# Performance work log

Measured on AMD Instinct MI355X. Metric: run time of the kernel, lower is better.

## Reference

```python
import jax, jax.numpy as jnp
import numpy as np

L, D, H, HK, DH, F, V, T, B = 8, 1024, 16, 4, 64, 2816, 32000, 1024, 2
G = H // HK
THETA = 10000.0
EPS = 1e-6
SCALE = DH ** -0.5


def _rope_tables(t, dh, theta):
    inv = 1.0 / theta ** (jnp.arange(0, dh, 2, dtype=jnp.float32) / dh)  # [dh/2]
    ang = jnp.arange(t, dtype=jnp.float32)[:, None] * inv[None, :]       # [T, dh/2]
    return jnp.cos(ang), jnp.sin(ang)


def _apply_rope(x, cos, sin):
    # x: [B, T, h, DH] -> rotate pairs (even, odd)
    xr = x.reshape(*x.shape[:-1], DH // 2, 2)
    x0, x1 = xr[..., 0], xr[..., 1]
    c = cos[None, :, None, :]
    s = sin[None, :, None, :]
    out = jnp.stack([x0 * c - x1 * s, x0 * s + x1 * c], axis=-1)
    return out.reshape(*x.shape)


def _rmsnorm(x, w):
    var = jnp.mean(x * x, axis=-1, keepdims=True)
    return x * jax.lax.rsqrt(var + EPS) * w


def setup_inputs() -> dict:
    key = jax.random.key(0)
    ks = jax.random.split(key, 10)
    s = 0.02
    return {
        "ids": jax.random.randint(ks[0], (B, T), 0, V),
        "emb": jax.random.normal(ks[1], (V, D), jnp.float32) * s,
        "qw": jax.random.normal(ks[2], (L, H * DH, D), jnp.float32) * s,
        "kw": jax.random.normal(ks[3], (L, HK * DH, D), jnp.float32) * s,
        "vw": jax.random.normal(ks[4], (L, HK * DH, D), jnp.float32) * s,
        "ow": jax.random.normal(ks[5], (L, D, D), jnp.float32) * s,
        "w1": jax.random.normal(ks[6], (L, F, D), jnp.float32) * s,
        "w2": jax.random.normal(ks[7], (L, D, F), jnp.float32) * s,
        "w3": jax.random.normal(ks[8], (L, F, D), jnp.float32) * s,
        "n1": jnp.ones((L, D), jnp.float32),
        "n2": jnp.ones((L, D), jnp.float32),
        "nf": jnp.ones((D,), jnp.float32),
    }


def _forward(ids, emb, qw, kw, vw, ow, w1, w2, w3, n1, n2, nf):
    cos, sin = _rope_tables(T, DH, THETA)
    causal = jnp.tril(jnp.ones((T, T), dtype=bool))  # [T, T]
    x = emb[ids]  # [B, T, D]
    for l in range(L):
        xn = _rmsnorm(x, n1[l])
        q = jnp.einsum("btd,ed->bte", xn, qw[l]).reshape(B, T, H, DH)
        k = jnp.einsum("btd,ed->bte", xn, kw[l]).reshape(B, T, HK, DH)
        v = jnp.einsum("btd,ed->bte", xn, vw[l]).reshape(B, T, HK, DH)
        q = _apply_rope(q, cos, sin)
        k = _apply_rope(k, cos, sin)
        # GQA: group query heads over shared kv heads
        qg = q.transpose(0, 2, 1, 3).reshape(B, HK, G, T, DH)
        kh = k.transpose(0, 2, 1, 3)  # [B, HK, T, DH]
        vh = v.transpose(0, 2, 1, 3)
        scores = jnp.einsum("bkgtd,bksd->bkgts", qg, kh) * SCALE
        scores = jnp.where(causal, scores, -jnp.inf)
        p = jax.nn.softmax(scores, axis=-1)
        out = jnp.einsum("bkgts,bksd->bkgtd", p, vh)
        out = out.reshape(B, H, T, DH).transpose(0, 2, 1, 3).reshape(B, T, D)
        x = x + jnp.einsum("btd,ed->bte", out, ow[l])
        xn2 = _rmsnorm(x, n2[l])
        h1 = jnp.einsum("btd,fd->btf", xn2, w1[l])
        h3 = jnp.einsum("btd,fd->btf", xn2, w3[l])
        x = x + jnp.einsum("btf,df->btd", jax.nn.silu(h1) * h3, w2[l])
    x = _rmsnorm(x, nf)
    logits = jnp.einsum("btd,vd->btv", x, emb)  # tied lm_head
    return logits


def reference(ids, emb, qw, kw, vw, ow, w1, w2, w3, n1, n2, nf):
    return _forward(ids, emb, qw, kw, vw, ow, w1, w2, w3, n1, n2, nf)
```

## Files before the change

kernel.cpp:

```cpp
#include <hip/hip_runtime.h>
#include <math.h>

#define L_ 8
#define D_ 1024
#define H_ 16
#define HK_ 4
#define DH_ 64
#define F_ 2816
#define V_ 32000
#define T_ 1024
#define B_ 2
#define M_ (B_*T_)
#define SCALE_ 0.125f

typedef unsigned short u16;
typedef unsigned int   u32;
typedef __attribute__((ext_vector_type(4))) float  f32x4;
typedef __attribute__((ext_vector_type(8))) short  bf16x8;
typedef __attribute__((ext_vector_type(4))) unsigned short u16x4;
typedef __attribute__((ext_vector_type(4))) unsigned int   u32x4;

__device__ __forceinline__ float bf2f(u16 h) {
    union { u32 u; float f; } v; v.u = ((u32)h) << 16; return v.f;
}
__device__ __forceinline__ u16 f2bf(float f) {
    union { float f; u32 u; } v; v.f = f;
    u32 r = v.u + 0x7fffu + ((v.u >> 16) & 1u);
    return (u16)(r >> 16);
}

__device__ __forceinline__ void gl_lds16(const void* g, void* l) {
    __builtin_amdgcn_global_load_lds(
        (const __attribute__((address_space(1))) unsigned int*)g,
        (__attribute__((address_space(3))) unsigned int*)l,
        16, 0, 0);
}

template<int BM, int EPI>
__global__ __launch_bounds__(256)
void gemm2_k(const u16* __restrict__ A, int K,
             const u16* __restrict__ W, int N,
             float* __restrict__ Of, u16* __restrict__ Ob)
{
    constexpr int FM = BM / 32;
    constexpr int FN = 4;
    constexpr int GM = M_ / BM;
    constexpr int IPA = BM / 64;
    __shared__ u16 sA[2 * BM * 32];
    __shared__ u16 sB[2 * 128 * 32];

    const int tid  = threadIdx.x;
    const int lane = tid & 63, wv = tid >> 6;
    const int wm = wv >> 1, wn = wv & 1;
    const int l15 = lane & 15, lhi = lane >> 4;
    const int m0 = wm * (BM / 2), n0 = wn * 64;

    const int nwg = gridDim.x;
    const int q8 = nwg >> 3, r8 = nwg & 7;
    const int xcd = blockIdx.x & 7, off8 = blockIdx.x >> 3;
    const int wgid = (xcd < r8 ? xcd * (q8 + 1) : r8 * (q8 + 1) + (xcd - r8) * q8) + off8;
    const int tM = wgid % GM, tN = wgid / GM;

    const int srow = lane >> 2;
    const int scol = (lane & 3) * 8;

    const u16* Abase = A + (size_t)(tM * BM) * K;
    const u16* Wbase = W + (size_t)(tN * 128) * K;

    f32x4 acc[FM][FN];
#pragma unroll
    for (int i = 0; i < FM; ++i)
#pragma unroll
        for (int j = 0; j < FN; ++j) acc[i][j] = f32x4{0.f, 0.f, 0.f, 0.f};

    auto stage = [&](int kt, int buf) {
        u16* sa = sA + buf * (BM * 32);
        u16* sb = sB + buf * (128 * 32);
#pragma unroll
        for (int i = 0; i < IPA; ++i) {
            int c = wv * IPA + i;
            gl_lds16(Abase + (size_t)(c * 16 + srow) * K + kt + scol, sa + c * 512);
        }
#pragma unroll
        for (int i = 0; i < 2; ++i) {
            int c = wv * 2 + i;
            gl_lds16(Wbase + (size_t)(c * 16 + srow) * K + kt + scol, sb + c * 512);
        }
    };

    const int nt = K >> 5;
    stage(0, 0);
    asm volatile("s_waitcnt vmcnt(0)" ::: "memory");
    __syncthreads();

    int cur = 0;
    for (int t = 0; t < nt; ++t) {
        if (t + 1 < nt) stage((t + 1) << 5, cur ^ 1);

        const u16* sa = sA + cur * (BM * 32);
        const u16* sb = sB + cur * (128 * 32);
        bf16x8 av[FM], bv[FN];
#pragma unroll
        for (int i = 0; i < FM; ++i)
            av[i] = *(const bf16x8*)&sa[(m0 + i * 16 + l15) * 32 + lhi * 8];
#pragma unroll
        for (int j = 0; j < FN; ++j)
            bv[j] = *(const bf16x8*)&sb[(n0 + j * 16 + l15) * 32 + lhi * 8];
#pragma unroll
        for (int i = 0; i < FM; ++i)
#pragma unroll
            for (int j = 0; j < FN; ++j)
                acc[i][j] = __builtin_amdgcn_mfma_f32_16x16x32_bf16(
                    av[i], bv[j], acc[i][j], 0, 0, 0);

        if (t + 1 < nt) {
            asm volatile("s_waitcnt vmcnt(0)" ::: "memory");
            __syncthreads();
            cur ^= 1;
        }
    }

#pragma unroll
    for (int i = 0; i < FM; ++i)
#pragma unroll
        for (int j = 0; j < FN; ++j) {
            size_t gm = (size_t)tM * BM + m0 + i * 16 + lhi * 4;
            size_t gn = (size_t)tN * 128 + n0 + j * 16 + l15;
#pragma unroll
            for (int r = 0; r < 4; ++r) {
                float v = acc[i][j][r];
                size_t idx = (gm + r) * (size_t)N + gn;
                if (EPI == 0)      Ob[idx] = f2bf(v);
                else if (EPI == 1) Of[idx] = v;
                else               Of[idx] += v;
            }
        }
}

__global__ __launch_bounds__(256)
void cvt_k(const float* __restrict__ src, u16* __restrict__ dst,
           unsigned long long sStride, unsigned long long dStride)
{
    int l = blockIdx.y;
    size_t i = ((size_t)blockIdx.x * 256 + threadIdx.x) * 4;
    f32x4 v = *(const f32x4*)(src + l * sStride + i);
    u16x4 o;
    o.x = f2bf(v.x); o.y = f2bf(v.y); o.z = f2bf(v.z); o.w = f2bf(v.w);
    *(u16x4*)(dst + l * dStride + i) = o;
}

template<int BM, int BN, int EPI, int NW>
__global__ __launch_bounds__(256)
void gemm_k(const u16* __restrict__ A, int K,
            const float* __restrict__ W0, const float* __restrict__ W1p,
            const float* __restrict__ W2p, int N0, int N1, int N,
            float* __restrict__ Of, u16* __restrict__ Ob)
{
    constexpr int FM = BM / 32;
    constexpr int FN = BN / 32;
    constexpr int LS = 40;
    __shared__ u16 sA[BM * LS];
    __shared__ u16 sB[BN * LS];

    const int tid  = threadIdx.x;
    const int lane = tid & 63, wv = tid >> 6;
    const int wm = wv >> 1, wn = wv & 1;
    const int l15 = lane & 15, lhi = lane >> 4;
    const int m0 = wm * (BM / 2), n0 = wn * (BN / 2);
    const int tM = blockIdx.y, tN = blockIdx.x;

    f32x4 acc[FM][FN];
#pragma unroll
    for (int i = 0; i < FM; ++i)
#pragma unroll
        for (int j = 0; j < FN; ++j) acc[i][j] = f32x4{0.f, 0.f, 0.f, 0.f};

    for (int kt = 0; kt < K; kt += 32) {
#pragma unroll
        for (int i = 0; i < BM / 64; ++i) {
            int cid = tid + i * 256;
            int row = cid >> 2, kc = cid & 3;
            const u16* src = A + (size_t)(tM * BM + row) * K + kt + kc * 8;
            *(u32x4*)&sA[row * LS + kc * 8] = *(const u32x4*)src;
        }
#pragma unroll
        for (int i = 0; i < BN / 32; ++i) {
            int cid = tid + i * 256;
            int row = cid >> 3, kc = cid & 7;
            int n = tN * BN + row;
            const float* wr;
            if (NW == 1)      wr = W0 + (size_t)n * K;
            else if (NW == 2) wr = (n < N0) ? (W0 + (size_t)n * K)
                                            : (W1p + (size_t)(n - N0) * K);
            else              wr = (n < N0) ? (W0 + (size_t)n * K)
                               : (n < N0 + N1) ? (W1p + (size_t)(n - N0) * K)
                                               : (W2p + (size_t)(n - N0 - N1) * K);
            f32x4 v = *(const f32x4*)(wr + kt + kc * 4);
            u16x4 o;
            o.x = f2bf(v.x); o.y = f2bf(v.y); o.z = f2bf(v.z); o.w = f2bf(v.w);
            *(u16x4*)&sB[row * LS + kc * 4] = o;
        }
        __syncthreads();

        bf16x8 av[FM], bv[FN];
#pragma unroll
        for (int i = 0; i < FM; ++i)
            av[i] = *(const bf16x8*)&sA[(m0 + i * 16 + l15) * LS + lhi * 8];
#pragma unroll
        for (int j = 0; j < FN; ++j)
            bv[j] = *(const bf16x8*)&sB[(n0 + j * 16 + l15) * LS + lhi * 8];
#pragma unroll
        for (int i = 0; i < FM; ++i)
#pragma unroll
            for (int j = 0; j < FN; ++j)
                acc[i][j] = __builtin_amdgcn_mfma_f32_16x16x32_bf16(
                    av[i], bv[j], acc[i][j], 0, 0, 0);
        __syncthreads();
    }

#pragma unroll
    for (int i = 0; i < FM; ++i)
#pragma unroll
        for (int j = 0; j < FN; ++j) {
            size_t gm = (size_t)tM * BM + m0 + i * 16 + lhi * 4;
            size_t gn = (size_t)tN * BN + n0 + j * 16 + l15;
#pragma unroll
            for (int r = 0; r < 4; ++r) {
                float v = acc[i][j][r];
                size_t idx = (gm + r) * (size_t)N + gn;
                if (EPI == 0)      Ob[idx] = f2bf(v);
                else if (EPI == 1) Of[idx] = v;
                else               Of[idx] += v;
            }
        }
}

__global__ __launch_bounds__(256)
void attn_k(const u16* __restrict__ qkv, u16* __restrict__ attn)
{
    const int qt = blockIdx.x, h = blockIdx.y, b = blockIdx.z;
    const int hk = h >> 2;
    const int tid = threadIdx.x;
    const int lane = tid & 63, w = tid >> 6;
    const int l15 = lane & 15, lhi = lane >> 4;
    __shared__ u16 sK[64 * 72];
    __shared__ u16 sVT[64 * 72];
    __shared__ u16 sP[4 * 16 * 72];

    const int q0 = qt * 64;
    const u16* qptr = qkv + (size_t)(b * T_ + q0 + w * 16 + l15) * 1536 + h * 64 + lhi * 8;
    bf16x8 aq0 = *(const bf16x8*)qptr;
    bf16x8 aq1 = *(const bf16x8*)(qptr + 32);

    f32x4 accO[4];
#pragma unroll
    for (int d = 0; d < 4; ++d) accO[d] = f32x4{0.f, 0.f, 0.f, 0.f};
    float m_r[4] = {-1e30f, -1e30f, -1e30f, -1e30f};
    float l_r[4] = {0.f, 0.f, 0.f, 0.f};
    const int myq = q0 + w * 16 + lhi * 4;
    u16* sPw = sP + w * 16 * 72;

    for (int kt = 0; kt <= qt; ++kt) {
#pragma unroll
        for (int i = 0; i < 2; ++i) {
            int cid = tid + i * 256;
            int r = cid >> 3, kc = cid & 7;
            const u16* src = qkv + (size_t)(b * T_ + kt * 64 + r) * 1536 + 1024 + hk * 64 + kc * 8;
            *(u32x4*)&sK[r * 72 + kc * 8] = *(const u32x4*)src;
        }
#pragma unroll
        for (int i = 0; i < 2; ++i) {
            int cid = tid + i * 256;
            int tt = cid >> 3, dc = cid & 7;
            const u16* src = qkv + (size_t)(b * T_ + kt * 64 + tt) * 1536 + 1280 + hk * 64 + dc * 8;
            bf16x8 vv = *(const bf16x8*)src;
#pragma unroll
            for (int j = 0; j < 8; ++j) sVT[(dc * 8 + j) * 72 + tt] = (u16)vv[j];
        }
        __syncthreads();

        f32x4 accS[4];
#pragma unroll
        for (int nf = 0; nf < 4; ++nf) accS[nf] = f32x4{0.f, 0.f, 0.f, 0.f};
#pragma unroll
        for (int s = 0; s < 2; ++s) {
            bf16x8 aqs = s ? aq1 : aq0;
#pragma unroll
            for (int nf = 0; nf < 4; ++nf) {
                bf16x8 bk = *(const bf16x8*)&sK[(nf * 16 + l15) * 72 + s * 32 + lhi * 8];
                accS[nf] = __builtin_amdgcn_mfma_f32_16x16x32_bf16(aqs, bk, accS[nf], 0, 0, 0);
            }
        }
#pragma unroll
        for (int nf = 0; nf < 4; ++nf)
#pragma unroll
            for (int r = 0; r < 4; ++r) {
                float v = accS[nf][r] * SCALE_;
                if (kt == qt) {
                    int kp = kt * 64 + nf * 16 + l15;
                    if (kp > myq + r) v = -1e30f;
                }
                accS[nf][r] = v;
            }
        float sc[4];
#pragma unroll
        for (int r = 0; r < 4; ++r) {
            float mx = fmaxf(fmaxf(accS[0][r], accS[1][r]), fmaxf(accS[2][r], accS[3][r]));
#pragma unroll
            for (int off = 1; off < 16; off <<= 1) mx = fmaxf(mx, __shfl_xor(mx, off));
            float mn = fmaxf(m_r[r], mx);
            sc[r] = expf(m_r[r] - mn);
            m_r[r] = mn;
        }
        float rs[4] = {0.f, 0.f, 0.f, 0.f};
#pragma unroll
        for (int nf = 0; nf < 4; ++nf)
#pragma unroll
            for (int r = 0; r < 4; ++r) {
                float p = expf(accS[nf][r] - m_r[r]);
                accS[nf][r] = p;
                rs[r] += p;
            }
#pragma unroll
        for (int r = 0; r < 4; ++r) {
#pragma unroll
            for (int off = 1; off < 16; off <<= 1) rs[r] += __shfl_xor(rs[r], off);
            l_r[r] = l_r[r] * sc[r] + rs[r];
        }
#pragma unroll
        for (int d = 0; d < 4; ++d)
#pragma unroll
            for (int r = 0; r < 4; ++r) accO[d][r] *= sc[r];

#pragma unroll
        for (int nf = 0; nf < 4; ++nf)
#pragma unroll
            for (int r = 0; r < 4; ++r)
                sPw[(lhi * 4 + r) * 72 + nf * 16 + l15] = f2bf(accS[nf][r]);
        bf16x8 pa0 = *(const bf16x8*)&sPw[l15 * 72 + lhi * 8];
        bf16x8 pa1 = *(const bf16x8*)&sPw[l15 * 72 + 32 + lhi * 8];
#pragma unroll
        for (int s = 0; s < 2; ++s) {
            bf16x8 pas = s ? pa1 : pa0;
#pragma unroll
            for (int d = 0; d < 4; ++d) {
                bf16x8 bvv = *(const bf16x8*)&sVT[(d * 16 + l15) * 72 + s * 32 + lhi * 8];
                accO[d] = __builtin_amdgcn_mfma_f32_16x16x32_bf16(pas, bvv, accO[d], 0, 0, 0);
            }
        }
        __syncthreads();
    }

#pragma unroll
    for (int d = 0; d < 4; ++d)
#pragma unroll
        for (int r = 0; r < 4; ++r) {
            int row = q0 + w * 16 + lhi * 4 + r;
            float o = accO[d][r] / l_r[r];
            attn[(size_t)(b * T_ + row) * 1024 + h * 64 + d * 16 + l15] = f2bf(o);
        }
}

__global__ __launch_bounds__(256)
void gather_k(const int* __restrict__ ids, const float* __restrict__ emb,
              float* __restrict__ x)
{
    int m = blockIdx.x, tid = threadIdx.x;
    int id = ids[m];
    *(f32x4*)(x + (size_t)m * D_ + tid * 4) =
        *(const f32x4*)(emb + (size_t)id * D_ + tid * 4);
}

__global__ __launch_bounds__(256)
void rmsnorm_k(const float* __restrict__ x, const float* __restrict__ g,
               u16* __restrict__ out)
{
    const int row = blockIdx.x, tid = threadIdx.x;
    const float* xr = x + (size_t)row * D_;
    f32x4 v = *(const f32x4*)(xr + tid * 4);
    float ss = v.x * v.x + v.y * v.y + v.z * v.z + v.w * v.w;
#pragma unroll
    for (int off = 32; off >= 1; off >>= 1) ss += __shfl_xor(ss, off);
    __shared__ float red[4];
    if ((tid & 63) == 0) red[tid >> 6] = ss;
    __syncthreads();
    float tot = red[0] + red[1] + red[2] + red[3];
    float rr = rsqrtf(tot * (1.0f / D_) + 1e-6f);
    f32x4 wv = *(const f32x4*)(g + tid * 4);
    u16x4 o;
    o.x = f2bf(v.x * rr * wv.x); o.y = f2bf(v.y * rr * wv.y);
    o.z = f2bf(v.z * rr * wv.z); o.w = f2bf(v.w * rr * wv.w);
    *(u16x4*)(out + (size_t)row * D_ + tid * 4) = o;
}

__global__ __launch_bounds__(256)
void rope_tab_k(float* __restrict__ tc, float* __restrict__ ts)
{
    int idx = blockIdx.x * 256 + threadIdx.x;
    int t = idx >> 5, j = idx & 31;
    float inv = powf(10000.0f, -(float)j * (1.0f / 32.0f));
    float ang = (float)t * inv;
    tc[idx] = cosf(ang);
    ts[idx] = sinf(ang);
}

__global__ __launch_bounds__(256)
void rope_k(u16* __restrict__ qkv, const float* __restrict__ tc,
            const float* __restrict__ ts)
{
    int idx = blockIdx.x * 256 + threadIdx.x;
    int m = idx / 160;
    int c = idx - m * 160;
    int t = m & (T_ - 1);
    int col = (c < 128) ? (c * 8) : (1024 + (c - 128) * 8);
    int j0 = (col & 63) >> 1;
    f32x4 cv = *(const f32x4*)(tc + t * 32 + j0);
    f32x4 sv = *(const f32x4*)(ts + t * 32 + j0);
    u16* p = qkv + (size_t)m * 1536 + col;
    bf16x8 v = *(const bf16x8*)p;
    bf16x8 o;
#pragma unroll
    for (int i = 0; i < 4; ++i) {
        float x0 = bf2f((u16)v[2 * i]), x1 = bf2f((u16)v[2 * i + 1]);
        o[2 * i]     = (short)f2bf(x0 * cv[i] - x1 * sv[i]);
        o[2 * i + 1] = (short)f2bf(x0 * sv[i] + x1 * cv[i]);
    }
    *(bf16x8*)p = o;
}

__global__ __launch_bounds__(256)
void silu_k(const u16* __restrict__ h13, u16* __restrict__ hh)
{
    int idx = blockIdx.x * 256 + threadIdx.x;
    int m = idx / 352;
    int c = idx - m * 352;
    const u16* h1p = h13 + (size_t)m * (2 * F_) + c * 8;
    bf16x8 a = *(const bf16x8*)h1p;
    bf16x8 b = *(const bf16x8*)(h1p + F_);
    bf16x8 o;
#pragma unroll
    for (int j = 0; j < 8; ++j) {
        float av = bf2f((u16)a[j]);
        float s = av / (1.0f + expf(-av));
        o[j] = (short)f2bf(s * bf2f((u16)b[j]));
    }
    *(bf16x8*)(hh + (size_t)m * F_ + c * 8) = o;
}

__global__ __launch_bounds__(256)
void silu_f32_k(const float* __restrict__ h13, u16* __restrict__ hh)
{
    int m = blockIdx.y;
    int f = blockIdx.x * 256 + threadIdx.x;
    float a = h13[(size_t)m * (2 * F_) + f];
    float c = h13[(size_t)m * (2 * F_) + F_ + f];
    float s = a / (1.0f + expf(-a));
    hh[(size_t)m * F_ + f] = f2bf(s * c);
}

__global__ __launch_bounds__(640)
void rope_slow_k(u16* __restrict__ qkv)
{
    int m = blockIdx.x;
    int c2 = threadIdx.x;
    int col = (c2 < 512) ? (c2 * 2) : (1024 + (c2 - 512) * 2);
    int d = col & 63;
    int t = m & (T_ - 1);
    float ang = (float)t * powf(10000.0f, -(float)d / 64.0f);
    float cs = cosf(ang), sn = sinf(ang);
    u16* p = qkv + (size_t)m * 1536 + col;
    float x0 = bf2f(p[0]), x1 = bf2f(p[1]);
    p[0] = f2bf(x0 * cs - x1 * sn);
    p[1] = f2bf(x0 * sn + x1 * cs);
}

extern "C" void kernel_launch(void* const* d_in, const int* in_sizes, int n_in,
                              void* d_out, int out_size, void* d_ws, size_t ws_size,
                              hipStream_t stream)
{
    const int*   ids = (const int*)d_in[0];
    const float* emb = (const float*)d_in[1];
    const float* qw  = (const float*)d_in[2];
    const float* kw  = (const float*)d_in[3];
    const float* vw  = (const float*)d_in[4];
    const float* ow  = (const float*)d_in[5];
    const float* w1  = (const float*)d_in[6];
    const float* w2  = (const float*)d_in[7];
    const float* w3  = (const float*)d_in[8];
    const float* n1  = (const float*)d_in[9];
    const float* n2  = (const float*)d_in[10];
    const float* nfw = (const float*)d_in[11];
    float* out = (float*)d_out;
    char*  ws  = (char*)d_ws;

    float* x    = (float*)(ws);
    u16*   xn   = (u16*)(ws + 8388608ULL);
    u16*   qkvb = (u16*)(ws + 12582912ULL);
    u16*   attnb= (u16*)(ws + 18874368ULL);
    u16*   h13  = (u16*)(ws + 23068672ULL);
    u16*   hh   = (u16*)(ws + 46137344ULL);
    float* ropec= (float*)(ws + 57671680ULL);
    float* ropes= (float*)(ws + 57802752ULL);
    u16*   embb = (u16*)(ws + 57933824ULL);
    u16*   wqkv = (u16*)(ws + 123469824ULL);
    u16*   wob  = (u16*)(ws + 148635648ULL);
    u16*   w13b = (u16*)(ws + 165412864ULL);
    u16*   w2b  = (u16*)(ws + 257687552ULL);
    const unsigned long long NEED = 303824896ULL;

    if (ws_size >= NEED) {
        cvt_k<<<dim3(32000, 1), 256, 0, stream>>>(emb, embb, 0, 0);
        cvt_k<<<dim3(1024, L_), 256, 0, stream>>>(qw, wqkv,            1048576ULL, 1572864ULL);
        cvt_k<<<dim3(256,  L_), 256, 0, stream>>>(kw, wqkv + 1048576,  262144ULL,  1572864ULL);
        cvt_k<<<dim3(256,  L_), 256, 0, stream>>>(vw, wqkv + 1310720,  262144ULL,  1572864ULL);
        cvt_k<<<dim3(1024, L_), 256, 0, stream>>>(ow, wob,             1048576ULL, 1048576ULL);
        cvt_k<<<dim3(2816, L_), 256, 0, stream>>>(w1, w13b,            2883584ULL, 5767168ULL);
        cvt_k<<<dim3(2816, L_), 256, 0, stream>>>(w3, w13b + 2883584,  2883584ULL, 5767168ULL);
        cvt_k<<<dim3(2816, L_), 256, 0, stream>>>(w2, w2b,             2883584ULL, 2883584ULL);
        rope_tab_k<<<T_ * 32 / 256, 256, 0, stream>>>(ropec, ropes);

        gather_k<<<M_, 256, 0, stream>>>(ids, emb, x);

        for (int l = 0; l < L_; ++l) {
            rmsnorm_k<<<M_, 256, 0, stream>>>(x, n1 + l * D_, xn);
            gemm2_k<64, 0><<<32 * 12, 256, 0, stream>>>(
                xn, D_, wqkv + (size_t)l * 1572864, 1536, nullptr, qkvb);
            rope_k<<<M_ * 160 / 256, 256, 0, stream>>>(qkvb, ropec, ropes);
            attn_k<<<dim3(T_ / 64, H_, B_), 256, 0, stream>>>(qkvb, attnb);
            gemm2_k<64, 2><<<32 * 8, 256, 0, stream>>>(
                attnb, D_, wob + (size_t)l * 1048576, 1024, x, nullptr);
            rmsnorm_k<<<M_, 256, 0, stream>>>(x, n2 + l * D_, xn);
            gemm2_k<128, 0><<<16 * 44, 256, 0, stream>>>(
                xn, D_, w13b + (size_t)l * 5767168, 2 * F_, nullptr, h13);
            silu_k<<<M_ * 352 / 256, 256, 0, stream>>>(h13, hh);
            gemm2_k<64, 2><<<32 * 8, 256, 0, stream>>>(
                hh, F_, w2b + (size_t)l * 2883584, 1024, x, nullptr);
        }

        rmsnorm_k<<<M_, 256, 0, stream>>>(x, nfw, xn);
        gemm2_k<128, 1><<<16 * 250, 256, 0, stream>>>(
            xn, D_, embb, V_, out, nullptr);
        return;
    }

    float* h13f = (float*)(ws + 23068672ULL);
    u16*   hhf  = (u16*)(ws + 69206016ULL);
    gather_k<<<M_, 256, 0, stream>>>(ids, emb, x);

    for (int l = 0; l < L_; ++l) {
        rmsnorm_k<<<M_, 256, 0, stream>>>(x, n1 + l * D_, xn);
        gemm_k<128, 64, 0, 3><<<dim3(24, 16), 256, 0, stream>>>(
            xn, D_,
            qw + (size_t)l * H_ * DH_ * D_,
            kw + (size_t)l * HK_ * DH_ * D_,
            vw + (size_t)l * HK_ * DH_ * D_,
            1024, 256, 1536, nullptr, qkvb);
        rope_slow_k<<<M_, 640, 0, stream>>>(qkvb);
        attn_k<<<dim3(T_ / 64, H_, B_), 256, 0, stream>>>(qkvb, attnb);
        gemm_k<128, 64, 2, 1><<<dim3(16, 16), 256, 0, stream>>>(
            attnb, D_, ow + (size_t)l * D_ * D_, nullptr, nullptr,
            0, 0, D_, x, nullptr);
        rmsnorm_k<<<M_, 256, 0, stream>>>(x, n2 + l * D_, xn);
        gemm_k<128, 128, 1, 2><<<dim3(44, 16), 256, 0, stream>>>(
            xn, D_, w1 + (size_t)l * F_ * D_, w3 + (size_t)l * F_ * D_, nullptr,
            F_, 0, 2 * F_, h13f, nullptr);
        silu_f32_k<<<dim3(11, M_), 256, 0, stream>>>(h13f, hhf);
        gemm_k<128, 64, 2, 1><<<dim3(16, 16), 256, 0, stream>>>(
            hhf, F_, w2 + (size_t)l * D_ * F_, nullptr, nullptr,
            0, 0, D_, x, nullptr);
    }

    rmsnorm_k<<<M_, 256, 0, stream>>>(x, nfw, xn);
    gemm_k<128, 128, 1, 1><<<dim3(250, 16), 256, 0, stream>>>(
        xn, D_, emb, nullptr, nullptr, 0, 0, V_, out, nullptr);
}
```

Measured before the change: 2.053 ms.

## Add 256x256 triple-buffered GEMM with fused SiLU-gate epilogue and interleaved W1/W3

Introduces a 512-thread 256x256-tile GEMM with three-stage global-to-LDS buffering, swizzled LDS layout and an XCD-aware block remap. It replaces both the gate/up GEMM and the LM-head GEMM. W1 and W3 rows are now interleaved at conversion time, so the new epilogue computes silu(h1)*h3 via a lane shuffle and writes the gated activation directly, which drops the separate silu kernel and the h13 intermediate round trip. The attention V-transpose LDS stride is padded from 72 to 74 to reduce bank conflicts. Larger tiles lower occupancy and raise register pressure, and the odd stride may misalign vector reads.

```diff
diff --git a/kernel.cpp b/kernel.cpp
--- a/kernel.cpp
+++ b/kernel.cpp
@@ -36,6 +36,135 @@
         16, 0, 0);
 }
 
+template<int EPI>
+__global__ __launch_bounds__(512, 2)
+void gemm8_k(const u16* __restrict__ A, int K,
+             const u16* __restrict__ W, int N,
+             float* __restrict__ Of, u16* __restrict__ Ob)
+{
+    __shared__ u16 sA[3 * 256 * 32];
+    __shared__ u16 sB[3 * 256 * 32];
+
+    const int tid  = threadIdx.x;
+    const int lane = tid & 63, wv = tid >> 6;
+    const int wm = wv >> 2, wn = wv & 3;
+    const int l15 = lane & 15, lhi = lane >> 4;
+    const int swl = (l15 & 3) ^ ((l15 >> 2) & 3);
+    const int psl = lhi ^ swl;
+
+    const int nwg = gridDim.x;
+    const int q8 = nwg >> 3;
+    const int xcd = blockIdx.x & 7, off8 = blockIdx.x >> 3;
+    const int wgid = xcd * q8 + off8;
+    const int tM = wgid & 7, tN = wgid >> 3;
+
+    const u16* Abase = A + (size_t)(tM * 256) * K;
+    const u16* Wbase = W + (size_t)(tN * 256) * K;
+
+    const int srow_in = lane >> 2;
+    const int spslot  = lane & 3;
+
+    f32x4 acc[8][4];
+#pragma unroll
+    for (int i = 0; i < 8; ++i)
+#pragma unroll
+        for (int j = 0; j < 4; ++j) acc[i][j] = f32x4{0.f, 0.f, 0.f, 0.f};
+
+    auto stageAB = [&](int t, int buf) {
+        u16* sa = sA + buf * (256 * 32);
+        u16* sb = sB + buf * (256 * 32);
+        const int kt = t << 5;
+#pragma unroll
+        for (int i = 0; i < 2; ++i) {
+            int c = wv * 2 + i;
+            int row = c * 16 + srow_in;
+            int lslot = spslot ^ ((row & 3) ^ ((row >> 2) & 3));
+            gl_lds16(Abase + (size_t)row * K + kt + lslot * 8, sa + c * 512);
+            gl_lds16(Wbase + (size_t)row * K + kt + lslot * 8, sb + c * 512);
+        }
+    };
+
+    const int nt = K >> 5;
+    stageAB(0, 0);
+    stageAB(1, 1);
+
+    for (int t = 0; t < nt; ++t) {
+        if (t + 2 < nt) {
+            stageAB(t + 2, (t + 2) % 3);
+            asm volatile("s_waitcnt vmcnt(8)" ::: "memory");
+        } else if (t + 1 < nt) {
+            asm volatile("s_waitcnt vmcnt(4)" ::: "memory");
+        } else {
+            asm volatile("s_waitcnt vmcnt(0)" ::: "memory");
+        }
+        __syncthreads();
+
+        const u16* sa = sA + (t % 3) * (256 * 32);
+        const u16* sb = sB + (t % 3) * (256 * 32);
+
+        bf16x8 bv[4];
+#pragma unroll
+        for (int j = 0; j < 4; ++j) {
+            int row = wn * 64 + j * 16 + l15;
+            bv[j] = *(const bf16x8*)&sb[row * 32 + psl * 8];
+        }
+        {
+            bf16x8 av[4];
+#pragma unroll
+            for (int i = 0; i < 4; ++i) {
+                int row = wm * 128 + i * 16 + l15;
+                av[i] = *(const bf16x8*)&sa[row * 32 + psl * 8];
+            }
+            __builtin_amdgcn_s_setprio(1);
+#pragma unroll
+            for (int i = 0; i < 4; ++i)
+#pragma unroll
+                for (int j = 0; j < 4; ++j)
+                    acc[i][j] = __builtin_amdgcn_mfma_f32_16x16x32_bf16(
+                        av[i], bv[j], acc[i][j], 0, 0, 0);
+            __builtin_amdgcn_s_setprio(0);
+        }
+        {
+            bf16x8 av[4];
+#pragma unroll
+            for (int i = 0; i < 4; ++i) {
+                int row = wm * 128 + (i + 4) * 16 + l15;
+                av[i] = *(const bf16x8*)&sa[row * 32 + psl * 8];
+            }
+            __builtin_amdgcn_s_setprio(1);
+#pragma unroll
+            for (int i = 0; i < 4; ++i)
+#pragma unroll
+                for (int j = 0; j < 4; ++j)
+                    acc[i + 4][j] = __builtin_amdgcn_mfma_f32_16x16x32_bf16(
+                        av[i], bv[j], acc[i + 4][j], 0, 0, 0);
+            __builtin_amdgcn_s_setprio(0);
+        }
+        __syncthreads();
+    }
+
+#pragma unroll
+    for (int i = 0; i < 8; ++i)
+#pragma unroll
+        for (int j = 0; j < 4; ++j) {
+            size_t gm = (size_t)tM * 256 + wm * 128 + i * 16 + lhi * 4;
+            size_t gn = (size_t)tN * 256 + wn * 64 + j * 16 + l15;
+#pragma unroll
+            for (int r = 0; r < 4; ++r) {
+                float v = acc[i][j][r];
+                if (EPI == 1) {
+                    Of[(gm + r) * (size_t)N + gn] = v;
+                } else {
+                    float b = __shfl_xor(v, 1);
+                    if ((lane & 1) == 0) {
+                        float s = v / (1.0f + expf(-v));
+                        Ob[(gm + r) * (size_t)F_ + (gn >> 1)] = f2bf(s * b);
+                    }
+                }
+            }
+        }
+}
+
 template<int BM, int EPI>
 __global__ __launch_bounds__(256)
 void gemm2_k(const u16* __restrict__ A, int K,
@@ -147,6 +276,18 @@
     u16x4 o;
     o.x = f2bf(v.x); o.y = f2bf(v.y); o.z = f2bf(v.z); o.w = f2bf(v.w);
     *(u16x4*)(dst + l * dStride + i) = o;
+}
+
+__global__ __launch_bounds__(256)
+void cvt_il_k(const float* __restrict__ src, u16* __restrict__ dst,
+              unsigned long long sStride, unsigned long long dStride, int off)
+{
+    int f = blockIdx.x, l = blockIdx.y;
+    int i = threadIdx.x * 4;
+    f32x4 v = *(const f32x4*)(src + l * sStride + (size_t)f * D_ + i);
+    u16x4 o;
+    o.x = f2bf(v.x); o.y = f2bf(v.y); o.z = f2bf(v.z); o.w = f2bf(v.w);
+    *(u16x4*)(dst + l * dStride + (size_t)(2 * f + off) * D_ + i) = o;
 }
 
 template<int BM, int BN, int EPI, int NW>
@@ -244,7 +385,7 @@
     const int lane = tid & 63, w = tid >> 6;
     const int l15 = lane & 15, lhi = lane >> 4;
     __shared__ u16 sK[64 * 72];
-    __shared__ u16 sVT[64 * 72];
+    __shared__ u16 sVT[64 * 74];
     __shared__ u16 sP[4 * 16 * 72];
 
     const int q0 = qt * 64;
@@ -275,7 +416,7 @@
             const u16* src = qkv + (size_t)(b * T_ + kt * 64 + tt) * 1536 + 1280 + hk * 64 + dc * 8;
             bf16x8 vv = *(const bf16x8*)src;
 #pragma unroll
-            for (int j = 0; j < 8; ++j) sVT[(dc * 8 + j) * 72 + tt] = (u16)vv[j];
+            for (int j = 0; j < 8; ++j) sVT[(dc * 8 + j) * 74 + tt] = (u16)vv[j];
         }
         __syncthreads();
 
@@ -344,7 +485,7 @@
             bf16x8 pas = s ? pa1 : pa0;
 #pragma unroll
             for (int d = 0; d < 4; ++d) {
-                bf16x8 bvv = *(const bf16x8*)&sVT[(d * 16 + l15) * 72 + s * 32 + lhi * 8];
+                bf16x8 bvv = *(const bf16x8*)&sVT[(d * 16 + l15) * 74 + s * 32 + lhi * 8];
                 accO[d] = __builtin_amdgcn_mfma_f32_16x16x32_bf16(pas, bvv, accO[d], 0, 0, 0);
             }
         }
@@ -426,25 +567,6 @@
         o[2 * i + 1] = (short)f2bf(x0 * sv[i] + x1 * cv[i]);
     }
     *(bf16x8*)p = o;
-}
-
-__global__ __launch_bounds__(256)
-void silu_k(const u16* __restrict__ h13, u16* __restrict__ hh)
-{
-    int idx = blockIdx.x * 256 + threadIdx.x;
-    int m = idx / 352;
-    int c = idx - m * 352;
-    const u16* h1p = h13 + (size_t)m * (2 * F_) + c * 8;
-    bf16x8 a = *(const bf16x8*)h1p;
-    bf16x8 b = *(const bf16x8*)(h1p + F_);
-    bf16x8 o;
-#pragma unroll
-    for (int j = 0; j < 8; ++j) {
-        float av = bf2f((u16)a[j]);
-        float s = av / (1.0f + expf(-av));
-        o[j] = (short)f2bf(s * bf2f((u16)b[j]));
-    }
-    *(bf16x8*)(hh + (size_t)m * F_ + c * 8) = o;
 }
 
 __global__ __launch_bounds__(256)
@@ -497,7 +619,6 @@
     u16*   xn   = (u16*)(ws + 8388608ULL);
     u16*   qkvb = (u16*)(ws + 12582912ULL);
     u16*   attnb= (u16*)(ws + 18874368ULL);
-    u16*   h13  = (u16*)(ws + 23068672ULL);
     u16*   hh   = (u16*)(ws + 46137344ULL);
     float* ropec= (float*)(ws + 57671680ULL);
     float* ropes= (float*)(ws + 57802752ULL);
@@ -514,8 +635,8 @@
         cvt_k<<<dim3(256,  L_), 256, 0, stream>>>(kw, wqkv + 1048576,  262144ULL,  1572864ULL);
         cvt_k<<<dim3(256,  L_), 256, 0, stream>>>(vw, wqkv + 1310720,  262144ULL,  1572864ULL);
         cvt_k<<<dim3(1024, L_), 256, 0, stream>>>(ow, wob,             1048576ULL, 1048576ULL);
-        cvt_k<<<dim3(2816, L_), 256, 0, stream>>>(w1, w13b,            2883584ULL, 5767168ULL);
-        cvt_k<<<dim3(2816, L_), 256, 0, stream>>>(w3, w13b + 2883584,  2883584ULL, 5767168ULL);
+        cvt_il_k<<<dim3(2816, L_), 256, 0, stream>>>(w1, w13b, 2883584ULL, 5767168ULL, 0);
+        cvt_il_k<<<dim3(2816, L_), 256, 0, stream>>>(w3, w13b, 2883584ULL, 5767168ULL, 1);
         cvt_k<<<dim3(2816, L_), 256, 0, stream>>>(w2, w2b,             2883584ULL, 2883584ULL);
         rope_tab_k<<<T_ * 32 / 256, 256, 0, stream>>>(ropec, ropes);
 
@@ -530,15 +651,14 @@
             gemm2_k<64, 2><<<32 * 8, 256, 0, stream>>>(
                 attnb, D_, wob + (size_t)l * 1048576, 1024, x, nullptr);
             rmsnorm_k<<<M_, 256, 0, stream>>>(x, n2 + l * D_, xn);
-            gemm2_k<128, 0><<<16 * 44, 256, 0, stream>>>(
-                xn, D_, w13b + (size_t)l * 5767168, 2 * F_, nullptr, h13);
-            silu_k<<<M_ * 352 / 256, 256, 0, stream>>>(h13, hh);
+            gemm8_k<3><<<8 * 22, 512, 0, stream>>>(
+                xn, D_, w13b + (size_t)l * 5767168, 5632, nullptr, hh);
             gemm2_k<64, 2><<<32 * 8, 256, 0, stream>>>(
                 hh, F_, w2b + (size_t)l * 2883584, 1024, x, nullptr);
         }
 
         rmsnorm_k<<<M_, 256, 0, stream>>>(x, nfw, xn);
-        gemm2_k<128, 1><<<16 * 250, 256, 0, stream>>>(
+        gemm8_k<1><<<8 * 125, 512, 0, stream>>>(
             xn, D_, embb, V_, out, nullptr);
         return;
     }
```

Result: slower. 2.340 ms (+13.9%).

## Pre-transpose V globally and rewrite attention with 128-key tiles and async LDS loads

Applied to the files above, without the earlier changes.

Adds a kernel that writes V transposed into a workspace buffer once per layer. A new attention kernel then uses 128-key tiles with XOR-swizzled LDS, loaded through direct global-to-LDS copies, and skips causally masked 32-key sub-blocks. This removes the per-block scalar transpose of V into shared memory and halves the number of tile iterations and barriers. The cost is an extra kernel launch, extra workspace, and more LDS per block, which may lower occupancy. The old attention kernel's padding also changes, but that kernel is no longer launched.

```diff
diff --git a/kernel.cpp b/kernel.cpp
--- a/kernel.cpp
+++ b/kernel.cpp
@@ -236,6 +236,187 @@
 }
 
 __global__ __launch_bounds__(256)
+void vtrans_k(const u16* __restrict__ qkv, u16* __restrict__ vt)
+{
+    int rr = blockIdx.x;
+    int d = rr & 63, hk = (rr >> 6) & 3, b = rr >> 8;
+    int t = threadIdx.x * 4;
+    const u16* base = qkv + (size_t)(b * T_ + t) * 1536 + 1280 + hk * 64 + d;
+    u16 a0 = base[0];
+    u16 a1 = base[1536];
+    u16 a2 = base[3072];
+    u16 a3 = base[4608];
+    u16x4 o; o.x = a0; o.y = a1; o.z = a2; o.w = a3;
+    *(u16x4*)(vt + (size_t)rr * T_ + t) = o;
+}
+
+__global__ __launch_bounds__(256)
+void attn2_k(const u16* __restrict__ qkv, const u16* __restrict__ vt,
+             u16* __restrict__ attn)
+{
+    const int qt = blockIdx.x, h = blockIdx.y, b = blockIdx.z;
+    const int hk = h >> 2;
+    const int tid = threadIdx.x;
+    const int lane = tid & 63, w = tid >> 6;
+    const int l15 = lane & 15, lhi = lane >> 4;
+
+    __shared__ u16 sK[128 * 64];
+    __shared__ u16 sVT[64 * 128];
+    __shared__ u16 sP[4][16 * 136];
+
+    const int q0 = qt * 64;
+    const u16* qptr = qkv + (size_t)(b * T_ + q0 + w * 16 + l15) * 1536 + h * 64 + lhi * 8;
+    bf16x8 aq0 = *(const bf16x8*)qptr;
+    bf16x8 aq1 = *(const bf16x8*)(qptr + 32);
+
+    f32x4 accO[4];
+#pragma unroll
+    for (int d = 0; d < 4; ++d) accO[d] = f32x4{0.f, 0.f, 0.f, 0.f};
+    float m_r[4] = {-1e30f, -1e30f, -1e30f, -1e30f};
+    float l_r[4] = {0.f, 0.f, 0.f, 0.f};
+    const int myq = q0 + w * 16 + lhi * 4;
+    const int qmaxw = q0 + w * 16 + 15;
+    u16* sPw = sP[w];
+
+    const int ntiles = (qt + 2) >> 1;
+    const u16* vtb = vt + (size_t)((b * HK_ + hk) * DH_) * T_;
+    const int L = lane;
+
+    for (int kt = 0; kt < ntiles; ++kt) {
+        const int t0 = kt * 128;
+#pragma unroll
+        for (int i = 0; i < 4; ++i) {
+            int c = w * 4 + i;
+            int row = c * 8 + (L >> 3);
+            int p = L & 7;
+            const u16* src = qkv + (size_t)(b * T_ + t0 + row) * 1536 + 1024 + hk * 64
+                             + ((p ^ (row & 7)) * 8);
+            gl_lds16(src, sK + c * 512);
+        }
+#pragma unroll
+        for (int i = 0; i < 4; ++i) {
+            int c = w * 4 + i;
+            int row = c * 4 + (L >> 4);
+            int p = L & 15;
+            const u16* src = vtb + (size_t)row * T_ + t0 + ((p ^ (row & 15)) * 8);
+            gl_lds16(src, sVT + c * 512);
+        }
+        asm volatile("s_waitcnt vmcnt(0)" ::: "memory");
+        __syncthreads();
+
+        const bool lastt = (kt == ntiles - 1);
+
+        f32x4 accS[8];
+#pragma unroll
+        for (int nf = 0; nf < 8; ++nf)
+            accS[nf] = f32x4{-1e30f, -1e30f, -1e30f, -1e30f};
+#pragma unroll
+        for (int pk = 0; pk < 4; ++pk) {
+            if (t0 + pk * 32 > qmaxw) continue;
+            f32x4 s0 = f32x4{0.f, 0.f, 0.f, 0.f};
+            f32x4 s1 = f32x4{0.f, 0.f, 0.f, 0.f};
+#pragma unroll
+            for (int kk = 0; kk < 2; ++kk) {
+                bf16x8 aqs = kk ? aq1 : aq0;
+                int r0 = (pk * 2) * 16 + l15;
+                int r1 = (pk * 2 + 1) * 16 + l15;
+                int ls = kk * 4 + lhi;
+                bf16x8 b0 = *(const bf16x8*)&sK[r0 * 64 + ((ls ^ (r0 & 7)) * 8)];
+                bf16x8 b1 = *(const bf16x8*)&sK[r1 * 64 + ((ls ^ (r1 & 7)) * 8)];
+                s0 = __builtin_amdgcn_mfma_f32_16x16x32_bf16(aqs, b0, s0, 0, 0, 0);
+                s1 = __builtin_amdgcn_mfma_f32_16x16x32_bf16(aqs, b1, s1, 0, 0, 0);
+            }
+#pragma unroll
+            for (int r = 0; r < 4; ++r) {
+                float v0 = s0[r] * SCALE_;
+                float v1 = s1[r] * SCALE_;
+                if (lastt) {
+                    int kp0 = t0 + (pk * 2) * 16 + l15;
+                    int kp1 = kp0 + 16;
+                    if (kp0 > myq + r) v0 = -1e30f;
+                    if (kp1 > myq + r) v1 = -1e30f;
+                }
+                accS[pk * 2][r] = v0;
+                accS[pk * 2 + 1][r] = v1;
+            }
+        }
+
+        float sc[4];
+#pragma unroll
+        for (int r = 0; r < 4; ++r) {
+            float mx = accS[0][r];
+#pragma unroll
+            for (int nf = 1; nf < 8; ++nf) mx = fmaxf(mx, accS[nf][r]);
+#pragma unroll
+            for (int off = 1; off < 16; off <<= 1) mx = fmaxf(mx, __shfl_xor(mx, off));
+            float mn = fmaxf(m_r[r], mx);
+            sc[r] = expf(m_r[r] - mn);
+            m_r[r] = mn;
+        }
+        float rs[4] = {0.f, 0.f, 0.f, 0.f};
+#pragma unroll
+        for (int pk = 0; pk < 4; ++pk) {
+            if (t0 + pk * 32 > qmaxw) continue;
+#pragma unroll
+            for (int g = 0; g < 2; ++g) {
+                int nf = pk * 2 + g;
+#pragma unroll
+                for (int r = 0; r < 4; ++r) {
+                    float p = expf(accS[nf][r] - m_r[r]);
+                    accS[nf][r] = p;
+                    rs[r] += p;
+                }
+            }
+        }
+#pragma unroll
+        for (int r = 0; r < 4; ++r) {
+#pragma unroll
+            for (int off = 1; off < 16; off <<= 1) rs[r] += __shfl_xor(rs[r], off);
+            l_r[r] = l_r[r] * sc[r] + rs[r];
+        }
+#pragma unroll
+        for (int d = 0; d < 4; ++d)
+#pragma unroll
+            for (int r = 0; r < 4; ++r) accO[d][r] *= sc[r];
+
+#pragma unroll
+        for (int pk = 0; pk < 4; ++pk) {
+            if (t0 + pk * 32 > qmaxw) continue;
+#pragma unroll
+            for (int g = 0; g < 2; ++g) {
+                int nf = pk * 2 + g;
+#pragma unroll
+                for (int r = 0; r < 4; ++r)
+                    sPw[(lhi * 4 + r) * 136 + nf * 16 + l15] = f2bf(accS[nf][r]);
+            }
+        }
+
+#pragma unroll
+        for (int kk = 0; kk < 4; ++kk) {
+            if (t0 + kk * 32 > qmaxw) continue;
+            bf16x8 pas = *(const bf16x8*)&sPw[l15 * 136 + kk * 32 + lhi * 8];
+#pragma unroll
+            for (int nf = 0; nf < 4; ++nf) {
+                int row = nf * 16 + l15;
+                int ls = kk * 4 + lhi;
+                bf16x8 bvv = *(const bf16x8*)&sVT[row * 128 + ((ls ^ (row & 15)) * 8)];
+                accO[nf] = __builtin_amdgcn_mfma_f32_16x16x32_bf16(pas, bvv, accO[nf], 0, 0, 0);
+            }
+        }
+        __syncthreads();
+    }
+
+#pragma unroll
+    for (int d = 0; d < 4; ++d)
+#pragma unroll
+        for (int r = 0; r < 4; ++r) {
+            int row = q0 + w * 16 + lhi * 4 + r;
+            float o = accO[d][r] / l_r[r];
+            attn[(size_t)(b * T_ + row) * 1024 + h * 64 + d * 16 + l15] = f2bf(o);
+        }
+}
+
+__global__ __launch_bounds__(256)
 void attn_k(const u16* __restrict__ qkv, u16* __restrict__ attn)
 {
     const int qt = blockIdx.x, h = blockIdx.y, b = blockIdx.z;
@@ -244,7 +425,7 @@
     const int lane = tid & 63, w = tid >> 6;
     const int l15 = lane & 15, lhi = lane >> 4;
     __shared__ u16 sK[64 * 72];
-    __shared__ u16 sVT[64 * 72];
+    __shared__ u16 sVT[64 * 74];
     __shared__ u16 sP[4 * 16 * 72];
 
     const int q0 = qt * 64;
@@ -275,7 +456,7 @@
             const u16* src = qkv + (size_t)(b * T_ + kt * 64 + tt) * 1536 + 1280 + hk * 64 + dc * 8;
             bf16x8 vv = *(const bf16x8*)src;
 #pragma unroll
-            for (int j = 0; j < 8; ++j) sVT[(dc * 8 + j) * 72 + tt] = (u16)vv[j];
+            for (int j = 0; j < 8; ++j) sVT[(dc * 8 + j) * 74 + tt] = (u16)vv[j];
         }
         __syncthreads();
 
@@ -344,7 +525,7 @@
             bf16x8 pas = s ? pa1 : pa0;
 #pragma unroll
             for (int d = 0; d < 4; ++d) {
-                bf16x8 bvv = *(const bf16x8*)&sVT[(d * 16 + l15) * 72 + s * 32 + lhi * 8];
+                bf16x8 bvv = *(const bf16x8*)&sVT[(d * 16 + l15) * 74 + s * 32 + lhi * 8];
                 accO[d] = __builtin_amdgcn_mfma_f32_16x16x32_bf16(pas, bvv, accO[d], 0, 0, 0);
             }
         }
@@ -506,7 +687,8 @@
     u16*   wob  = (u16*)(ws + 148635648ULL);
     u16*   w13b = (u16*)(ws + 165412864ULL);
     u16*   w2b  = (u16*)(ws + 257687552ULL);
-    const unsigned long long NEED = 303824896ULL;
+    u16*   vtb  = (u16*)(ws + 303824896ULL);
+    const unsigned long long NEED = 304873472ULL;
 
     if (ws_size >= NEED) {
         cvt_k<<<dim3(32000, 1), 256, 0, stream>>>(emb, embb, 0, 0);
@@ -526,7 +708,8 @@
             gemm2_k<64, 0><<<32 * 12, 256, 0, stream>>>(
                 xn, D_, wqkv + (size_t)l * 1572864, 1536, nullptr, qkvb);
             rope_k<<<M_ * 160 / 256, 256, 0, stream>>>(qkvb, ropec, ropes);
-            attn_k<<<dim3(T_ / 64, H_, B_), 256, 0, stream>>>(qkvb, attnb);
+            vtrans_k<<<B_ * HK_ * DH_, 256, 0, stream>>>(qkvb, vtb);
+            attn2_k<<<dim3(T_ / 64, H_, B_), 256, 0, stream>>>(qkvb, vtb, attnb);
             gemm2_k<64, 2><<<32 * 8, 256, 0, stream>>>(
                 attnb, D_, wob + (size_t)l * 1048576, 1024, x, nullptr);
             rmsnorm_k<<<M_, 256, 0, stream>>>(x, n2 + l * D_, xn);
```

After: 1.987 ms. -3.2%, faster.
